# Optimization experiments

Measured on AMD Instinct MI355X. Metric: run time of the kernel, lower is better.

Reference implementation:

```python
import jax, jax.numpy as jnp
import numpy as np

BETA_2 = 1.0
LAMBDA_2 = 1.0


def _segment_logsumexp(x, seg, num_segments):
    # numerically stable segment logsumexp; empty segments -> 0.0
    m = jax.ops.segment_max(x, seg, num_segments=num_segments)
    m_safe = jnp.where(jnp.isfinite(m), m, 0.0)
    s = jax.ops.segment_sum(jnp.exp(x - m_safe[seg]), seg, num_segments=num_segments)
    lse = m_safe + jnp.log(s)
    return jnp.where(s > 0, lse, 0.0)


def setup_inputs() -> dict:
    key = jax.random.key(0)
    k1, k2, k3, k4, k5 = jax.random.split(key, 5)
    num_nodes, d, num_edges, num_graphs = 100000, 64, 3200000, 256
    Q2 = jax.random.normal(k1, (num_nodes, d), dtype=jnp.float32)
    K2 = jax.random.normal(k2, (num_nodes, d), dtype=jnp.float32)
    c_2 = jax.random.randint(k3, (num_edges,), 0, num_nodes)
    u_2 = jax.random.randint(k4, (num_edges,), 0, num_nodes)
    batch = jnp.sort(jax.random.randint(k5, (num_nodes,), 0, num_graphs))
    return {"Q2": Q2, "K2": K2, "c_2": c_2, "u_2": u_2, "batch": batch,
            "num_graphs": num_graphs}


def reference(Q2, K2, c_2, u_2, batch, num_graphs):
    num_nodes, d = Q2.shape
    scale = d ** 0.5
    # pairwise dot over edges: [E]
    ell_2 = jnp.sum(Q2[c_2] * K2[u_2], axis=-1) / scale
    # segment logsumexp grouped by destination node c: [N]
    lse_2 = _segment_logsumexp(BETA_2 * ell_2, c_2, num_nodes)
    # scatter-add per-node lse into per-graph energy: [G]
    graph_lse = jax.ops.segment_sum(lse_2, batch, num_segments=num_graphs)
    E = (LAMBDA_2 / BETA_2) * graph_lse
    return E
```

## Files before the change

### kernel.cpp

```cpp
#include <hip/hip_runtime.h>
#include <hip/hip_fp8.h>
#include <math.h>

typedef __attribute__((ext_vector_type(2))) float fv2;

#if defined(__has_builtin)
#  if __has_builtin(__builtin_amdgcn_cvt_pk_f32_fp8) && \
      __has_builtin(__builtin_amdgcn_cvt_pk_fp8_f32)
#    define PE_HAVE_FP8_BUILTINS 1
#  endif
#endif

#define MAX_NB 512
#define MAX_NB2 2048
#define UQ 4
#define NPB 256
#define NPB_SHIFT 8
#define B2_EPT 16
#define B2_CHUNK (B2_EPT * 256)
#define RT 1024

__device__ __forceinline__ unsigned pack4_fp8(float a, float b, float c, float d) {
#ifdef PE_HAVE_FP8_BUILTINS
    int w = 0;
    w = __builtin_amdgcn_cvt_pk_fp8_f32(a, b, w, false);
    w = __builtin_amdgcn_cvt_pk_fp8_f32(c, d, w, true);
    return (unsigned)w;
#else
    unsigned r = 0;
    r |= (unsigned)__hip_fp8_e4m3(a).__x;
    r |= (unsigned)__hip_fp8_e4m3(b).__x << 8;
    r |= (unsigned)__hip_fp8_e4m3(c).__x << 16;
    r |= (unsigned)__hip_fp8_e4m3(d).__x << 24;
    return r;
#endif
}

__device__ __forceinline__ float dot4w_fp8(unsigned qa, unsigned ka, float acc) {
#ifdef PE_HAVE_FP8_BUILTINS
    fv2 q0 = __builtin_amdgcn_cvt_pk_f32_fp8((int)qa, false);
    fv2 q1 = __builtin_amdgcn_cvt_pk_f32_fp8((int)qa, true);
    fv2 k0 = __builtin_amdgcn_cvt_pk_f32_fp8((int)ka, false);
    fv2 k1 = __builtin_amdgcn_cvt_pk_f32_fp8((int)ka, true);
    acc = fmaf(q0.x, k0.x, acc);
    acc = fmaf(q0.y, k0.y, acc);
    acc = fmaf(q1.x, k1.x, acc);
    acc = fmaf(q1.y, k1.y, acc);
    return acc;
#else
#pragma unroll
    for (int j = 0; j < 4; ++j) {
        __hip_fp8_e4m3 qv, kv;
        qv.__x = (qa >> (8 * j)) & 0xff;
        kv.__x = (ka >> (8 * j)) & 0xff;
        acc = fmaf((float)qv, (float)kv, acc);
    }
    return acc;
#endif
}

__device__ __forceinline__ float dot16_fp8(const uint4& q, const uint4& k) {
    float d = 0.0f;
    d = dot4w_fp8(q.x, k.x, d);
    d = dot4w_fp8(q.y, k.y, d);
    d = dot4w_fp8(q.z, k.z, d);
    d = dot4w_fp8(q.w, k.w, d);
    return d;
}

__device__ __forceinline__ float red4(float d) {
    d += __shfl_xor(d, 1, 64);
    d += __shfl_xor(d, 2, 64);
    return d;
}

__device__ __forceinline__ int uquarter(int uu, int t1, int t2, int t3) {
    return (uu >= t1) + (uu >= t2) + (uu >= t3);
}

__global__ __launch_bounds__(256) void pe_convcount_kernel(
    const float* __restrict__ Q,
    const float* __restrict__ K,
    unsigned* __restrict__ Qq,
    unsigned* __restrict__ Kq,
    float* __restrict__ node_sum,
    float* __restrict__ out,
    const int* __restrict__ c,
    const int* __restrict__ u,
    unsigned* __restrict__ cnt,
    int n4, int num_nodes, int num_graphs, int num_edges,
    int nb2p, int nblk, int nconv,
    int t1, int t2, int t3) {
    __shared__ unsigned h[MAX_NB2];
    const int tid = threadIdx.x;

    if (blockIdx.x < nconv) {
        const int i = blockIdx.x * 256 + tid;
        if (i < num_nodes) node_sum[i] = 0.0f;
        if (i < num_graphs) out[i] = 0.0f;
        if (i >= n4) return;
        const float4 q = ((const float4*)Q)[i];
        const float4 k = ((const float4*)K)[i];
        Qq[i] = pack4_fp8(q.x, q.y, q.z, q.w);
        Kq[i] = pack4_fp8(k.x, k.y, k.z, k.w);
        return;
    }

    const int blk = blockIdx.x - nconv;
    for (int b = tid; b < MAX_NB2; b += 256) h[b] = 0u;
    __syncthreads();

    const int estart = blk * B2_CHUNK;
    const int ecount = min(B2_CHUNK, num_edges - estart);
    const int n4e = ecount >> 2;
    const int4* c4 = (const int4*)(c + estart);
    const int4* u4 = (const int4*)(u + estart);
    for (int k = tid; k < n4e; k += 256) {
        const int4 cv = c4[k];
        const int4 uv = u4[k];
        atomicAdd(&h[(cv.x >> NPB_SHIFT) * UQ + uquarter(uv.x, t1, t2, t3)], 1u);
        atomicAdd(&h[(cv.y >> NPB_SHIFT) * UQ + uquarter(uv.y, t1, t2, t3)], 1u);
        atomicAdd(&h[(cv.z >> NPB_SHIFT) * UQ + uquarter(uv.z, t1, t2, t3)], 1u);
        atomicAdd(&h[(cv.w >> NPB_SHIFT) * UQ + uquarter(uv.w, t1, t2, t3)], 1u);
    }
    for (int e = (n4e << 2) + tid; e < ecount; e += 256) {
        const int cc = c[estart + e];
        const int uu = u[estart + e];
        atomicAdd(&h[(cc >> NPB_SHIFT) * UQ + uquarter(uu, t1, t2, t3)], 1u);
    }
    __syncthreads();

    for (int b = tid; b < nb2p; b += 256)
        cnt[(size_t)blk * nb2p + b] = h[b];
}

__global__ __launch_bounds__(256) void pe_matscan_kernel(
    unsigned* __restrict__ cnt,
    unsigned* __restrict__ bin_cnt,
    int nblk, int nb2p) {
    __shared__ unsigned wsum[4][16];
    const int t = threadIdx.x;
    const int lane = t & 63;
    const int w = t >> 6;
    const int col0 = blockIdx.x * 16;

    unsigned carry[16];
#pragma unroll
    for (int i = 0; i < 16; ++i) carry[i] = 0u;

    for (int t0 = 0; t0 < nblk; t0 += 256) {
        const int blk = t0 + t;
        unsigned v[16], orig[16];
        if (blk < nblk) {
            const uint4* p = (const uint4*)(cnt + (size_t)blk * nb2p + col0);
            const uint4 a = p[0], b = p[1], cc = p[2], dd = p[3];
            v[0]=a.x;  v[1]=a.y;  v[2]=a.z;  v[3]=a.w;
            v[4]=b.x;  v[5]=b.y;  v[6]=b.z;  v[7]=b.w;
            v[8]=cc.x; v[9]=cc.y; v[10]=cc.z; v[11]=cc.w;
            v[12]=dd.x; v[13]=dd.y; v[14]=dd.z; v[15]=dd.w;
        } else {
#pragma unroll
            for (int i = 0; i < 16; ++i) v[i] = 0u;
        }
#pragma unroll
        for (int i = 0; i < 16; ++i) orig[i] = v[i];

#pragma unroll
        for (int off = 1; off < 64; off <<= 1) {
            unsigned nv[16];
#pragma unroll
            for (int i = 0; i < 16; ++i) nv[i] = __shfl_up(v[i], off, 64);
            if (lane >= off) {
#pragma unroll
                for (int i = 0; i < 16; ++i) v[i] += nv[i];
            }
        }
        if (lane == 63) {
#pragma unroll
            for (int i = 0; i < 16; ++i) wsum[w][i] = v[i];
        }
        __syncthreads();

        unsigned woff[16];
#pragma unroll
        for (int i = 0; i < 16; ++i) woff[i] = 0u;
        for (int ww = 0; ww < w; ++ww)
#pragma unroll
            for (int i = 0; i < 16; ++i) woff[i] += wsum[ww][i];

        if (blk < nblk) {
            uint4 o[4];
            unsigned e[16];
#pragma unroll
            for (int i = 0; i < 16; ++i) e[i] = carry[i] + woff[i] + v[i] - orig[i];
            o[0] = make_uint4(e[0], e[1], e[2], e[3]);
            o[1] = make_uint4(e[4], e[5], e[6], e[7]);
            o[2] = make_uint4(e[8], e[9], e[10], e[11]);
            o[3] = make_uint4(e[12], e[13], e[14], e[15]);
            uint4* p = (uint4*)(cnt + (size_t)blk * nb2p + col0);
            p[0] = o[0]; p[1] = o[1]; p[2] = o[2]; p[3] = o[3];
        }

#pragma unroll
        for (int i = 0; i < 16; ++i)
            carry[i] += wsum[0][i] + wsum[1][i] + wsum[2][i] + wsum[3][i];
        __syncthreads();
    }

    if (t == 0) {
#pragma unroll
        for (int i = 0; i < 16; ++i) bin_cnt[col0 + i] = carry[i];
    }
}

__global__ __launch_bounds__(1024) void pe_scan_kernel(
    const unsigned* __restrict__ bin_cnt,
    unsigned* __restrict__ bin_base,
    int nb2) {
    __shared__ unsigned s[1024];
    const int t = threadIdx.x;
    const int i0 = 2 * t, i1 = 2 * t + 1;
    const unsigned v0 = (i0 < nb2) ? bin_cnt[i0] : 0u;
    const unsigned v1 = (i1 < nb2) ? bin_cnt[i1] : 0u;
    const unsigned p = v0 + v1;
    s[t] = p;
    __syncthreads();
    for (int off = 1; off < 1024; off <<= 1) {
        const unsigned mine = s[t];
        const unsigned add = (t >= off) ? s[t - off] : 0u;
        __syncthreads();
        s[t] = mine + add;
        __syncthreads();
    }
    const unsigned excl = s[t] - p;
    if (i0 < nb2) bin_base[i0] = excl;
    if (i1 < nb2) bin_base[i1] = excl + v0;
    if (t == 1023) bin_base[nb2] = s[1023];
}

__global__ __launch_bounds__(256) void pe_binify_kernel(
    const int* __restrict__ c,
    const int* __restrict__ u,
    const unsigned* __restrict__ cnt,
    const unsigned* __restrict__ bin_base,
    unsigned* __restrict__ recs,
    int num_edges, int nb2, int nb2p, int nblk,
    int t1, int t2, int t3) {
    __shared__ unsigned rank[MAX_NB2];
    __shared__ unsigned lstart[MAX_NB2];
    __shared__ unsigned basesh[MAX_NB2];
    __shared__ unsigned srec[B2_CHUNK];
    __shared__ unsigned short sbuk[B2_CHUNK];
    __shared__ unsigned wtot[4];

    const int tid = threadIdx.x;
    const int blk = blockIdx.x;
    const int estart = blk * B2_CHUNK;
    const int ecount = min(B2_CHUNK, num_edges - estart);

    for (int b = tid; b < MAX_NB2; b += 256) rank[b] = 0u;
    for (int b = tid; b < nb2; b += 256)
        basesh[b] = bin_base[b] + cnt[(size_t)blk * nb2p + b];
    __syncthreads();

    unsigned rw[B2_EPT];
    int rb[B2_EPT];
    unsigned rr[B2_EPT];

    if (ecount == B2_CHUNK) {
        const int4* c4 = (const int4*)(c + estart);
        const int4* u4 = (const int4*)(u + estart);
#pragma unroll
        for (int jj = 0; jj < 4; ++jj) {
            const int k = jj * 256 + tid;
            const int4 cv = c4[k];
            const int4 uv = u4[k];
            const int j = jj * 4;
            rb[j + 0] = (cv.x >> NPB_SHIFT) * UQ + uquarter(uv.x, t1, t2, t3);
            rb[j + 1] = (cv.y >> NPB_SHIFT) * UQ + uquarter(uv.y, t1, t2, t3);
            rb[j + 2] = (cv.z >> NPB_SHIFT) * UQ + uquarter(uv.z, t1, t2, t3);
            rb[j + 3] = (cv.w >> NPB_SHIFT) * UQ + uquarter(uv.w, t1, t2, t3);
            rw[j + 0] = ((unsigned)uv.x << NPB_SHIFT) | (unsigned)(cv.x & (NPB - 1));
            rw[j + 1] = ((unsigned)uv.y << NPB_SHIFT) | (unsigned)(cv.y & (NPB - 1));
            rw[j + 2] = ((unsigned)uv.z << NPB_SHIFT) | (unsigned)(cv.z & (NPB - 1));
            rw[j + 3] = ((unsigned)uv.w << NPB_SHIFT) | (unsigned)(cv.w & (NPB - 1));
            rr[j + 0] = atomicAdd(&rank[rb[j + 0]], 1u);
            rr[j + 1] = atomicAdd(&rank[rb[j + 1]], 1u);
            rr[j + 2] = atomicAdd(&rank[rb[j + 2]], 1u);
            rr[j + 3] = atomicAdd(&rank[rb[j + 3]], 1u);
        }
    } else {
#pragma unroll
        for (int j = 0; j < B2_EPT; ++j) {
            rb[j] = -1;
            const int e = estart + j * 256 + tid;
            if (e < num_edges) {
                const int cc = c[e];
                const int uu = u[e];
                rb[j] = (cc >> NPB_SHIFT) * UQ + uquarter(uu, t1, t2, t3);
                rw[j] = ((unsigned)uu << NPB_SHIFT) | (unsigned)(cc & (NPB - 1));
                rr[j] = atomicAdd(&rank[rb[j]], 1u);
            }
        }
    }
    __syncthreads();

    {
        const int b8 = tid * 8;
        unsigned v[8];
        unsigned tsum = 0;
#pragma unroll
        for (int i = 0; i < 8; ++i) { v[i] = rank[b8 + i]; tsum += v[i]; }
        unsigned incl = tsum;
        const int lane = tid & 63;
#pragma unroll
        for (int off = 1; off < 64; off <<= 1) {
            const unsigned nv = __shfl_up(incl, off, 64);
            if (lane >= off) incl += nv;
        }
        if (lane == 63) wtot[tid >> 6] = incl;
        __syncthreads();
        unsigned woff = 0;
        const int w = tid >> 6;
        for (int i = 0; i < w; ++i) woff += wtot[i];
        unsigned run = woff + incl - tsum;
#pragma unroll
        for (int i = 0; i < 8; ++i) { lstart[b8 + i] = run; run += v[i]; }
    }
    __syncthreads();

#pragma unroll
    for (int j = 0; j < B2_EPT; ++j) {
        if (rb[j] >= 0) {
            const unsigned pos = lstart[rb[j]] + rr[j];
            srec[pos] = rw[j];
            sbuk[pos] = (unsigned short)rb[j];
        }
    }
    __syncthreads();

    for (int i = tid; i < ecount; i += 256) {
        const int b = sbuk[i];
        recs[basesh[b] + (unsigned)i - lstart[b]] = srec[i];
    }
}

__global__ __launch_bounds__(256) void pe_dotred_kernel(
    const unsigned* __restrict__ Qq,
    const unsigned* __restrict__ Kq,
    const unsigned* __restrict__ recs,
    const unsigned* __restrict__ bin_base,
    float* __restrict__ node_sum,
    int num_nodes, int nb) {
    __shared__ uint4 qlds[NPB * 4];
    __shared__ float acc[NPB];
    __shared__ unsigned rlds[RT];

    const int g = blockIdx.x;
    const int B = g >> 2;
    const int q = g & 3;
    if (B >= nb) return;

    const int t = threadIdx.x;
    const int gteam = t >> 2;
    const int sub = t & 3;
    const float inv_scale = 0.125f;

    const int nrows = min(NPB, num_nodes - B * NPB);
    const uint4* qsrc = (const uint4*)Qq + (size_t)B * NPB * 4;
    for (int i = t; i < nrows * 4; i += 256) qlds[i] = qsrc[i];
    acc[t] = 0.0f;

    const unsigned r0 = bin_base[B * UQ + q];
    const unsigned r1 = bin_base[B * UQ + q + 1];

    for (unsigned t0 = r0; t0 < r1; t0 += RT) {
        const unsigned n = min((unsigned)RT, r1 - t0);
        __syncthreads();
        for (unsigned i = t; i < n; i += 256) rlds[i] = recs[t0 + i];
        __syncthreads();
        for (unsigned i = gteam; i < n; i += 64) {
            const unsigned rec = rlds[i];
            const unsigned uu = rec >> NPB_SHIFT;
            const unsigned local = rec & (NPB - 1);
            const uint4 k = *(const uint4*)(Kq + (size_t)uu * 16 + sub * 4);
            const uint4 q4 = qlds[local * 4 + sub];
            const float d = red4(dot16_fp8(q4, k));
            if (sub == 0) atomicAdd(&acc[local], __expf(d * inv_scale));
        }
    }
    __syncthreads();

    if (t < nrows && acc[t] != 0.0f)
        atomicAdd(&node_sum[B * NPB + t], acc[t]);
}

__global__ __launch_bounds__(256) void pe_node_kernel(
    const float* __restrict__ node_sum,
    const int* __restrict__ batch,
    float* __restrict__ out,
    int num_nodes) {
    const int n = blockIdx.x * blockDim.x + threadIdx.x;
    const bool valid = (n < num_nodes);
    const int nc = valid ? n : (num_nodes - 1);

    const float s = valid ? node_sum[nc] : 0.0f;
    float lse = (s > 0.0f) ? logf(s) : 0.0f;
    if (!valid) lse = 0.0f;
    const int b = batch[nc];

    const int b0 = __shfl(b, 0, 64);
    const bool uniform = __all(b == b0);
    if (uniform) {
        lse += __shfl_xor(lse, 1, 64);
        lse += __shfl_xor(lse, 2, 64);
        lse += __shfl_xor(lse, 4, 64);
        lse += __shfl_xor(lse, 8, 64);
        lse += __shfl_xor(lse, 16, 64);
        lse += __shfl_xor(lse, 32, 64);
        if ((threadIdx.x & 63) == 0 && lse != 0.0f) {
            atomicAdd(&out[b0], lse);
        }
    } else {
        if (valid && lse != 0.0f) {
            atomicAdd(&out[b], lse);
        }
    }
}


__global__ __launch_bounds__(256) void pe_convert_kernel(
    const float* __restrict__ Q,
    const float* __restrict__ K,
    unsigned* __restrict__ Qq,
    unsigned* __restrict__ Kq,
    float* __restrict__ node_sum,
    float* __restrict__ out,
    int n4, int num_nodes, int num_graphs) {
    const int i = blockIdx.x * blockDim.x + threadIdx.x;
    if (i < num_nodes) node_sum[i] = 0.0f;
    if (i < num_graphs) out[i] = 0.0f;
    if (i >= n4) return;
    const float4 q = ((const float4*)Q)[i];
    const float4 k = ((const float4*)K)[i];
    Qq[i] = pack4_fp8(q.x, q.y, q.z, q.w);
    Kq[i] = pack4_fp8(k.x, k.y, k.z, k.w);
}

__global__ __launch_bounds__(256) void pe_edge_kernel(
    const unsigned* __restrict__ Qq,
    const unsigned* __restrict__ Kq,
    const int* __restrict__ c,
    const int* __restrict__ u,
    float* __restrict__ node_sum,
    int num_edges) {
    const int tid = blockIdx.x * blockDim.x + threadIdx.x;
    const int group = tid >> 2;
    const int sub = tid & 3;
    const int ngroups = (gridDim.x * blockDim.x) >> 2;
    const float inv_scale = 0.125f;

    const int E4 = num_edges & ~3;

    for (int base = group * 4; base < E4; base += ngroups * 4) {
        const int4 ci = *(const int4*)(c + base);
        const int4 ui = *(const int4*)(u + base);

        const uint4 q0 = *(const uint4*)(Qq + (size_t)ci.x * 16 + sub * 4);
        const uint4 q1 = *(const uint4*)(Qq + (size_t)ci.y * 16 + sub * 4);
        const uint4 q2 = *(const uint4*)(Qq + (size_t)ci.z * 16 + sub * 4);
        const uint4 q3 = *(const uint4*)(Qq + (size_t)ci.w * 16 + sub * 4);
        const uint4 k0 = *(const uint4*)(Kq + (size_t)ui.x * 16 + sub * 4);
        const uint4 k1 = *(const uint4*)(Kq + (size_t)ui.y * 16 + sub * 4);
        const uint4 k2 = *(const uint4*)(Kq + (size_t)ui.z * 16 + sub * 4);
        const uint4 k3 = *(const uint4*)(Kq + (size_t)ui.w * 16 + sub * 4);

        float d0 = red4(dot16_fp8(q0, k0));
        float d1 = red4(dot16_fp8(q1, k1));
        float d2 = red4(dot16_fp8(q2, k2));
        float d3 = red4(dot16_fp8(q3, k3));

        const float dsel = (sub == 0) ? d0 : (sub == 1) ? d1 : (sub == 2) ? d2 : d3;
        const int csel = (sub == 0) ? ci.x : (sub == 1) ? ci.y : (sub == 2) ? ci.z : ci.w;
        atomicAdd(&node_sum[csel], __expf(dsel * inv_scale));
    }

    for (int e = E4 + group; e < num_edges; e += ngroups) {
        const int cc = c[e];
        const int uu = u[e];
        const uint4 q = *(const uint4*)(Qq + (size_t)cc * 16 + sub * 4);
        const uint4 k = *(const uint4*)(Kq + (size_t)uu * 16 + sub * 4);
        float d = red4(dot16_fp8(q, k));
        if (sub == 0) atomicAdd(&node_sum[cc], __expf(d * inv_scale));
    }
}

extern "C" void kernel_launch(void* const* d_in, const int* in_sizes, int n_in,
                              void* d_out, int out_size, void* d_ws, size_t ws_size,
                              hipStream_t stream) {
    const float* Q2 = (const float*)d_in[0];
    const float* K2 = (const float*)d_in[1];
    const int* c_2 = (const int*)d_in[2];
    const int* u_2 = (const int*)d_in[3];
    const int* batch = (const int*)d_in[4];

    const int num_nodes = in_sizes[4];
    const int num_edges = in_sizes[2];
    const int num_graphs = out_size;
    const int d = in_sizes[0] / num_nodes;
    const size_t row_elems = (size_t)num_nodes * d;
    const size_t row_bytes = row_elems;

    const int nb = (num_nodes + NPB - 1) >> NPB_SHIFT;
    const int nb2 = nb * UQ;
    const int nb2p = (nb2 + 15) & ~15;
    const int nblk = (num_edges + B2_CHUNK - 1) / B2_CHUNK;

    const int t1 = num_nodes >> 2;
    const int t2 = num_nodes >> 1;
    const int t3 = t1 + t2;

    unsigned* Qq = (unsigned*)d_ws;
    unsigned* Kq = Qq + row_bytes / 4;
    unsigned* meta = Kq + row_bytes / 4;
    unsigned* bin_cnt = meta;
    unsigned* bin_base = meta + MAX_NB2;
    float* node_sum_b = (float*)(meta + 2 * MAX_NB2 + 16);
    const size_t ns_pad = ((size_t)num_nodes + 15) & ~(size_t)15;
    unsigned* recs = (unsigned*)node_sum_b + ns_pad;
    unsigned* cnt = recs + num_edges;
    float* node_sum_f = (float*)meta;
    float* out = (float*)d_out;

    const size_t need_binned = row_bytes * 2 + (size_t)(2 * MAX_NB2 + 16) * 4 +
                               ns_pad * 4 + (size_t)num_edges * 4 +
                               (size_t)nblk * nb2p * 4;
    const bool use_binned = (nb <= MAX_NB) && (ws_size >= need_binned) &&
                            (d == 64) && (num_nodes <= (1 << 23));

    float* node_sum = use_binned ? node_sum_b : node_sum_f;
    const int n4 = (int)(row_elems / 4);
    const int nconv = (n4 + 255) / 256;

    if (use_binned) {
        pe_convcount_kernel<<<nconv + nblk, 256, 0, stream>>>(
            Q2, K2, Qq, Kq, node_sum, out, c_2, u_2, cnt,
            n4, num_nodes, num_graphs, num_edges, nb2p, nblk, nconv,
            t1, t2, t3);
        pe_matscan_kernel<<<nb2p / 16, 256, 0, stream>>>(cnt, bin_cnt,
                                                         nblk, nb2p);
        pe_scan_kernel<<<1, 1024, 0, stream>>>(bin_cnt, bin_base, nb2);
        pe_binify_kernel<<<nblk, 256, 0, stream>>>(c_2, u_2, cnt,
                                                   bin_base, recs,
                                                   num_edges, nb2, nb2p, nblk,
                                                   t1, t2, t3);
        pe_dotred_kernel<<<nb * UQ, 256, 0, stream>>>(Qq, Kq, recs,
                                                      bin_base,
                                                      node_sum, num_nodes, nb);
    } else {
        pe_convert_kernel<<<nconv, 256, 0, stream>>>(
            Q2, K2, Qq, Kq, node_sum, out, n4, num_nodes, num_graphs);
        pe_edge_kernel<<<8192, 256, 0, stream>>>(Qq, Kq, c_2, u_2,
                                                 node_sum, num_edges);
    }

    {
        const int block = 256;
        const int grid = (num_nodes + block - 1) / block;
        pe_node_kernel<<<grid, block, 0, stream>>>(node_sum, batch, out,
                                                   num_nodes);
    }
}
```

Before: 222.9 us.

## Bin edges by destination block only and split each bin evenly across blocks

```diff
diff --git a/kernel.cpp b/kernel.cpp
--- a/kernel.cpp
+++ b/kernel.cpp
@@ -11,14 +11,12 @@
 #  endif
 #endif
 
-#define MAX_NB 512
-#define MAX_NB2 2048
-#define UQ 4
+#define MAX_NBP 512
 #define NPB 256
 #define NPB_SHIFT 8
 #define B2_EPT 16
 #define B2_CHUNK (B2_EPT * 256)
-#define RT 1024
+#define CPB 4
 
 __device__ __forceinline__ unsigned pack4_fp8(float a, float b, float c, float d) {
 #ifdef PE_HAVE_FP8_BUILTINS
@@ -74,10 +72,6 @@
     return d;
 }
 
-__device__ __forceinline__ int uquarter(int uu, int t1, int t2, int t3) {
-    return (uu >= t1) + (uu >= t2) + (uu >= t3);
-}
-
 __global__ __launch_bounds__(256) void pe_convcount_kernel(
     const float* __restrict__ Q,
     const float* __restrict__ K,
@@ -86,12 +80,10 @@
     float* __restrict__ node_sum,
     float* __restrict__ out,
     const int* __restrict__ c,
-    const int* __restrict__ u,
     unsigned* __restrict__ cnt,
     int n4, int num_nodes, int num_graphs, int num_edges,
-    int nb2p, int nblk, int nconv,
-    int t1, int t2, int t3) {
-    __shared__ unsigned h[MAX_NB2];
+    int nbp, int nblk, int nconv) {
+    __shared__ unsigned h[MAX_NBP];
     const int tid = threadIdx.x;
 
     if (blockIdx.x < nconv) {
@@ -107,37 +99,32 @@
     }
 
     const int blk = blockIdx.x - nconv;
-    for (int b = tid; b < MAX_NB2; b += 256) h[b] = 0u;
+    for (int b = tid; b < MAX_NBP; b += 256) h[b] = 0u;
     __syncthreads();
 
     const int estart = blk * B2_CHUNK;
     const int ecount = min(B2_CHUNK, num_edges - estart);
     const int n4e = ecount >> 2;
     const int4* c4 = (const int4*)(c + estart);
-    const int4* u4 = (const int4*)(u + estart);
     for (int k = tid; k < n4e; k += 256) {
-        const int4 cv = c4[k];
-        const int4 uv = u4[k];
-        atomicAdd(&h[(cv.x >> NPB_SHIFT) * UQ + uquarter(uv.x, t1, t2, t3)], 1u);
-        atomicAdd(&h[(cv.y >> NPB_SHIFT) * UQ + uquarter(uv.y, t1, t2, t3)], 1u);
-        atomicAdd(&h[(cv.z >> NPB_SHIFT) * UQ + uquarter(uv.z, t1, t2, t3)], 1u);
-        atomicAdd(&h[(cv.w >> NPB_SHIFT) * UQ + uquarter(uv.w, t1, t2, t3)], 1u);
-    }
-    for (int e = (n4e << 2) + tid; e < ecount; e += 256) {
-        const int cc = c[estart + e];
-        const int uu = u[estart + e];
-        atomicAdd(&h[(cc >> NPB_SHIFT) * UQ + uquarter(uu, t1, t2, t3)], 1u);
-    }
-    __syncthreads();
-
-    for (int b = tid; b < nb2p; b += 256)
-        cnt[(size_t)blk * nb2p + b] = h[b];
+        const int4 v = c4[k];
+        atomicAdd(&h[v.x >> NPB_SHIFT], 1u);
+        atomicAdd(&h[v.y >> NPB_SHIFT], 1u);
+        atomicAdd(&h[v.z >> NPB_SHIFT], 1u);
+        atomicAdd(&h[v.w >> NPB_SHIFT], 1u);
+    }
+    for (int e = (n4e << 2) + tid; e < ecount; e += 256)
+        atomicAdd(&h[c[estart + e] >> NPB_SHIFT], 1u);
+    __syncthreads();
+
+    for (int b = tid; b < nbp; b += 256)
+        cnt[(size_t)blk * nbp + b] = h[b];
 }
 
 __global__ __launch_bounds__(256) void pe_matscan_kernel(
     unsigned* __restrict__ cnt,
     unsigned* __restrict__ bin_cnt,
-    int nblk, int nb2p) {
+    int nblk, int nbp) {
     __shared__ unsigned wsum[4][16];
     const int t = threadIdx.x;
     const int lane = t & 63;
@@ -152,7 +139,7 @@
         const int blk = t0 + t;
         unsigned v[16], orig[16];
         if (blk < nblk) {
-            const uint4* p = (const uint4*)(cnt + (size_t)blk * nb2p + col0);
+            const uint4* p = (const uint4*)(cnt + (size_t)blk * nbp + col0);
             const uint4 a = p[0], b = p[1], cc = p[2], dd = p[3];
             v[0]=a.x;  v[1]=a.y;  v[2]=a.z;  v[3]=a.w;
             v[4]=b.x;  v[5]=b.y;  v[6]=b.z;  v[7]=b.w;
@@ -197,7 +184,7 @@
             o[1] = make_uint4(e[4], e[5], e[6], e[7]);
             o[2] = make_uint4(e[8], e[9], e[10], e[11]);
             o[3] = make_uint4(e[12], e[13], e[14], e[15]);
-            uint4* p = (uint4*)(cnt + (size_t)blk * nb2p + col0);
+            uint4* p = (uint4*)(cnt + (size_t)blk * nbp + col0);
             p[0] = o[0]; p[1] = o[1]; p[2] = o[2]; p[3] = o[3];
         }
 
@@ -216,14 +203,11 @@
 __global__ __launch_bounds__(1024) void pe_scan_kernel(
     const unsigned* __restrict__ bin_cnt,
     unsigned* __restrict__ bin_base,
-    int nb2) {
+    int nb) {
     __shared__ unsigned s[1024];
     const int t = threadIdx.x;
-    const int i0 = 2 * t, i1 = 2 * t + 1;
-    const unsigned v0 = (i0 < nb2) ? bin_cnt[i0] : 0u;
-    const unsigned v1 = (i1 < nb2) ? bin_cnt[i1] : 0u;
-    const unsigned p = v0 + v1;
-    s[t] = p;
+    const unsigned v = (t < nb) ? bin_cnt[t] : 0u;
+    s[t] = v;
     __syncthreads();
     for (int off = 1; off < 1024; off <<= 1) {
         const unsigned mine = s[t];
@@ -232,10 +216,8 @@
         s[t] = mine + add;
         __syncthreads();
     }
-    const unsigned excl = s[t] - p;
-    if (i0 < nb2) bin_base[i0] = excl;
-    if (i1 < nb2) bin_base[i1] = excl + v0;
-    if (t == 1023) bin_base[nb2] = s[1023];
+    if (t < nb) bin_base[t] = s[t] - v;
+    if (t == 0) bin_base[nb] = s[1023];
 }
 
 __global__ __launch_bounds__(256) void pe_binify_kernel(
@@ -244,11 +226,10 @@
     const unsigned* __restrict__ cnt,
     const unsigned* __restrict__ bin_base,
     unsigned* __restrict__ recs,
-    int num_edges, int nb2, int nb2p, int nblk,
-    int t1, int t2, int t3) {
-    __shared__ unsigned rank[MAX_NB2];
-    __shared__ unsigned lstart[MAX_NB2];
-    __shared__ unsigned basesh[MAX_NB2];
+    int num_edges, int nb, int nbp, int nblk) {
+    __shared__ unsigned rank[MAX_NBP];
+    __shared__ unsigned lstart[MAX_NBP];
+    __shared__ unsigned basesh[MAX_NBP];
     __shared__ unsigned srec[B2_CHUNK];
     __shared__ unsigned short sbuk[B2_CHUNK];
     __shared__ unsigned wtot[4];
@@ -258,9 +239,9 @@
     const int estart = blk * B2_CHUNK;
     const int ecount = min(B2_CHUNK, num_edges - estart);
 
-    for (int b = tid; b < MAX_NB2; b += 256) rank[b] = 0u;
-    for (int b = tid; b < nb2; b += 256)
-        basesh[b] = bin_base[b] + cnt[(size_t)blk * nb2p + b];
+    for (int b = tid; b < MAX_NBP; b += 256) rank[b] = 0u;
+    for (int b = tid; b < nb; b += 256)
+        basesh[b] = bin_base[b] + cnt[(size_t)blk * nbp + b];
     __syncthreads();
 
     unsigned rw[B2_EPT];
@@ -276,10 +257,10 @@
             const int4 cv = c4[k];
             const int4 uv = u4[k];
             const int j = jj * 4;
-            rb[j + 0] = (cv.x >> NPB_SHIFT) * UQ + uquarter(uv.x, t1, t2, t3);
-            rb[j + 1] = (cv.y >> NPB_SHIFT) * UQ + uquarter(uv.y, t1, t2, t3);
-            rb[j + 2] = (cv.z >> NPB_SHIFT) * UQ + uquarter(uv.z, t1, t2, t3);
-            rb[j + 3] = (cv.w >> NPB_SHIFT) * UQ + uquarter(uv.w, t1, t2, t3);
+            rb[j + 0] = cv.x >> NPB_SHIFT;
+            rb[j + 1] = cv.y >> NPB_SHIFT;
+            rb[j + 2] = cv.z >> NPB_SHIFT;
+            rb[j + 3] = cv.w >> NPB_SHIFT;
             rw[j + 0] = ((unsigned)uv.x << NPB_SHIFT) | (unsigned)(cv.x & (NPB - 1));
             rw[j + 1] = ((unsigned)uv.y << NPB_SHIFT) | (unsigned)(cv.y & (NPB - 1));
             rw[j + 2] = ((unsigned)uv.z << NPB_SHIFT) | (unsigned)(cv.z & (NPB - 1));
@@ -297,7 +278,7 @@
             if (e < num_edges) {
                 const int cc = c[e];
                 const int uu = u[e];
-                rb[j] = (cc >> NPB_SHIFT) * UQ + uquarter(uu, t1, t2, t3);
+                rb[j] = cc >> NPB_SHIFT;
                 rw[j] = ((unsigned)uu << NPB_SHIFT) | (unsigned)(cc & (NPB - 1));
                 rr[j] = atomicAdd(&rank[rb[j]], 1u);
             }
@@ -306,11 +287,10 @@
     __syncthreads();
 
     {
-        const int b8 = tid * 8;
-        unsigned v[8];
-        unsigned tsum = 0;
-#pragma unroll
-        for (int i = 0; i < 8; ++i) { v[i] = rank[b8 + i]; tsum += v[i]; }
+        const int b2 = tid * 2;
+        const unsigned v0 = rank[b2 + 0];
+        const unsigned v1 = rank[b2 + 1];
+        const unsigned tsum = v0 + v1;
         unsigned incl = tsum;
         const int lane = tid & 63;
 #pragma unroll
@@ -323,9 +303,9 @@
         unsigned woff = 0;
         const int w = tid >> 6;
         for (int i = 0; i < w; ++i) woff += wtot[i];
-        unsigned run = woff + incl - tsum;
-#pragma unroll
-        for (int i = 0; i < 8; ++i) { lstart[b8 + i] = run; run += v[i]; }
+        const unsigned run = woff + incl - tsum;
+        lstart[b2 + 0] = run;
+        lstart[b2 + 1] = run + v0;
     }
     __syncthreads();
 
@@ -354,11 +334,10 @@
     int num_nodes, int nb) {
     __shared__ uint4 qlds[NPB * 4];
     __shared__ float acc[NPB];
-    __shared__ unsigned rlds[RT];
 
     const int g = blockIdx.x;
     const int B = g >> 2;
-    const int q = g & 3;
+    const int chunk = g & 3;
     if (B >= nb) return;
 
     const int t = threadIdx.x;
@@ -370,24 +349,37 @@
     const uint4* qsrc = (const uint4*)Qq + (size_t)B * NPB * 4;
     for (int i = t; i < nrows * 4; i += 256) qlds[i] = qsrc[i];
     acc[t] = 0.0f;
-
-    const unsigned r0 = bin_base[B * UQ + q];
-    const unsigned r1 = bin_base[B * UQ + q + 1];
-
-    for (unsigned t0 = r0; t0 < r1; t0 += RT) {
-        const unsigned n = min((unsigned)RT, r1 - t0);
-        __syncthreads();
-        for (unsigned i = t; i < n; i += 256) rlds[i] = recs[t0 + i];
-        __syncthreads();
-        for (unsigned i = gteam; i < n; i += 64) {
-            const unsigned rec = rlds[i];
-            const unsigned uu = rec >> NPB_SHIFT;
-            const unsigned local = rec & (NPB - 1);
-            const uint4 k = *(const uint4*)(Kq + (size_t)uu * 16 + sub * 4);
-            const uint4 q4 = qlds[local * 4 + sub];
-            const float d = red4(dot16_fp8(q4, k));
-            if (sub == 0) atomicAdd(&acc[local], __expf(d * inv_scale));
-        }
+    __syncthreads();
+
+    const unsigned s0 = bin_base[B];
+    const unsigned len = bin_base[B + 1] - s0;
+    const unsigned r0 = s0 + (unsigned)(((unsigned long long)len * chunk) / CPB);
+    const unsigned r1 = s0 + (unsigned)(((unsigned long long)len * (chunk + 1)) / CPB);
+
+    unsigned i = r0 + gteam;
+    for (; i + 64 < r1; i += 128) {
+        const unsigned recA = recs[i];
+        const unsigned recB = recs[i + 64];
+        const unsigned uA = recA >> NPB_SHIFT, lA = recA & (NPB - 1);
+        const unsigned uB = recB >> NPB_SHIFT, lB = recB & (NPB - 1);
+        const uint4 kA = *(const uint4*)(Kq + (size_t)uA * 16 + sub * 4);
+        const uint4 kB = *(const uint4*)(Kq + (size_t)uB * 16 + sub * 4);
+        const uint4 qA = qlds[lA * 4 + sub];
+        const uint4 qB = qlds[lB * 4 + sub];
+        const float dA = red4(dot16_fp8(qA, kA));
+        const float dB = red4(dot16_fp8(qB, kB));
+        if (sub == 0) {
+            atomicAdd(&acc[lA], __expf(dA * inv_scale));
+            atomicAdd(&acc[lB], __expf(dB * inv_scale));
+        }
+    }
+    for (; i < r1; i += 64) {
+        const unsigned rec = recs[i];
+        const unsigned uu = rec >> NPB_SHIFT, ll = rec & (NPB - 1);
+        const uint4 k = *(const uint4*)(Kq + (size_t)uu * 16 + sub * 4);
+        const uint4 q4 = qlds[ll * 4 + sub];
+        const float d = red4(dot16_fp8(q4, k));
+        if (sub == 0) atomicAdd(&acc[ll], __expf(d * inv_scale));
     }
     __syncthreads();
 
@@ -512,30 +504,25 @@
     const size_t row_bytes = row_elems;
 
     const int nb = (num_nodes + NPB - 1) >> NPB_SHIFT;
-    const int nb2 = nb * UQ;
-    const int nb2p = (nb2 + 15) & ~15;
+    const int nbp = (nb + 15) & ~15;
     const int nblk = (num_edges + B2_CHUNK - 1) / B2_CHUNK;
-
-    const int t1 = num_nodes >> 2;
-    const int t2 = num_nodes >> 1;
-    const int t3 = t1 + t2;
 
     unsigned* Qq = (unsigned*)d_ws;
     unsigned* Kq = Qq + row_bytes / 4;
     unsigned* meta = Kq + row_bytes / 4;
     unsigned* bin_cnt = meta;
-    unsigned* bin_base = meta + MAX_NB2;
-    float* node_sum_b = (float*)(meta + 2 * MAX_NB2 + 16);
+    unsigned* bin_base = meta + MAX_NBP;
+    float* node_sum_b = (float*)(meta + 2 * MAX_NBP + 16);
     const size_t ns_pad = ((size_t)num_nodes + 15) & ~(size_t)15;
     unsigned* recs = (unsigned*)node_sum_b + ns_pad;
     unsigned* cnt = recs + num_edges;
     float* node_sum_f = (float*)meta;
     float* out = (float*)d_out;
 
-    const size_t need_binned = row_bytes * 2 + (size_t)(2 * MAX_NB2 + 16) * 4 +
+    const size_t need_binned = row_bytes * 2 + (size_t)(2 * MAX_NBP + 16) * 4 +
                                ns_pad * 4 + (size_t)num_edges * 4 +
-                               (size_t)nblk * nb2p * 4;
-    const bool use_binned = (nb <= MAX_NB) && (ws_size >= need_binned) &&
+                               (size_t)nblk * nbp * 4;
+    const bool use_binned = (nb <= MAX_NBP) && (ws_size >= need_binned) &&
                             (d == 64) && (num_nodes <= (1 << 23));
 
     float* node_sum = use_binned ? node_sum_b : node_sum_f;
@@ -544,19 +531,17 @@
 
     if (use_binned) {
         pe_convcount_kernel<<<nconv + nblk, 256, 0, stream>>>(
-            Q2, K2, Qq, Kq, node_sum, out, c_2, u_2, cnt,
-            n4, num_nodes, num_graphs, num_edges, nb2p, nblk, nconv,
-            t1, t2, t3);
-        pe_matscan_kernel<<<nb2p / 16, 256, 0, stream>>>(cnt, bin_cnt,
-                                                         nblk, nb2p);
-        pe_scan_kernel<<<1, 1024, 0, stream>>>(bin_cnt, bin_base, nb2);
+            Q2, K2, Qq, Kq, node_sum, out, c_2, cnt,
+            n4, num_nodes, num_graphs, num_edges, nbp, nblk, nconv);
+        pe_matscan_kernel<<<nbp / 16, 256, 0, stream>>>(cnt, bin_cnt,
+                                                        nblk, nbp);
+        pe_scan_kernel<<<1, 1024, 0, stream>>>(bin_cnt, bin_base, nb);
         pe_binify_kernel<<<nblk, 256, 0, stream>>>(c_2, u_2, cnt,
                                                    bin_base, recs,
-                                                   num_edges, nb2, nb2p, nblk,
-                                                   t1, t2, t3);
-        pe_dotred_kernel<<<nb * UQ, 256, 0, stream>>>(Qq, Kq, recs,
-                                                      bin_base,
-                                                      node_sum, num_nodes, nb);
+                                                   num_edges, nb, nbp, nblk);
+        pe_dotred_kernel<<<nb * CPB, 256, 0, stream>>>(Qq, Kq, recs,
+                                                       bin_base,
+                                                       node_sum, num_nodes, nb);
     } else {
         pe_convert_kernel<<<nconv, 256, 0, stream>>>(
             Q2, K2, Qq, Kq, node_sum, out, n4, num_nodes, num_graphs);
```

Result: faster. 204.0 us (-8.5%).
